# Optimization experiments

Hardware: AMD Instinct MI355X
Metric: run time of the kernel (lower is better)

The kernel has to match this reference:

```python
import jax, jax.numpy as jnp
import numpy as np

CAPACITY_FACTOR = 1.25  # config.capacity_factor


def setup_inputs() -> dict:
    key = jax.random.key(0)
    ks = jax.random.split(key, 5)
    B, S, D, F, E = 8, 2048, 768, 3072, 8
    return {
        "x": jax.random.normal(ks[0], (B, S, D), jnp.float32),
        "switch_w": jax.random.normal(ks[1], (D, E), jnp.float32) * 0.02,
        "switch_b": jnp.zeros((E,), jnp.float32),
        "w1": jax.random.normal(ks[2], (E, D, F), jnp.float32) * 0.02,
        "b1": jnp.zeros((E, F), jnp.float32),
        "w2": jax.random.normal(ks[3], (E, F, D), jnp.float32) * 0.02,
        "b2": jnp.zeros((E, D), jnp.float32),
    }


def reference(x, switch_w, switch_b, w1, b1, w2, b2):
    B, S, D = x.shape
    E = w1.shape[0]
    xf = x.reshape(-1, D)                      # [N, D] tokens
    N = xf.shape[0]
    capacity = int(CAPACITY_FACTOR * N / E)

    # top-1 switch routing
    probs = jax.nn.softmax(xf @ switch_w + switch_b, axis=-1)   # [N, E]
    prob_max = jnp.max(probs, axis=-1)                          # [N]
    routes = jnp.argmax(probs, axis=-1)                         # [N] int

    # priority drop: within each expert keep the `capacity` tokens with
    # highest gate prob. Rank tokens within their expert by descending prob.
    sort_idx = jnp.lexsort((-prob_max, routes))                 # [N]
    counts = jnp.bincount(routes, length=E)
    starts = jnp.concatenate([jnp.zeros((1,), counts.dtype), jnp.cumsum(counts)[:-1]])
    rank_sorted = jnp.arange(N) - starts[routes[sort_idx]]
    rank = jnp.zeros((N,), jnp.int32).at[sort_idx].set(rank_sorted.astype(jnp.int32))
    keep = rank < capacity

    # dispatch kept tokens into [E, capacity, D]; overflow goes to slot E
    dest_e = jnp.where(keep, routes, E)
    dest_c = jnp.where(keep, rank, 0)
    buf = jnp.zeros((E + 1, capacity, D), xf.dtype).at[dest_e, dest_c].set(xf)

    # per-expert FFN (grouped GEMM), GELU is exact (erf) as in nn.GELU()
    h = jax.nn.gelu(jnp.einsum('ecd,edf->ecf', buf[:E], w1) + b1[:, None, :],
                    approximate=False)
    o = jnp.einsum('ecf,efd->ecd', h, w2) + b2[:, None, :]      # [E, cap, D]

    # combine: kept tokens get expert output, dropped tokens pass through x
    y_exp = o[routes, dest_c]                                    # [N, D]
    y = jnp.where(keep[:, None], y_exp, xf)
    out = y * prob_max[:, None]                                  # is_scale_prob
    return out.reshape(B, S, D)
```

## Files before the change

kernel.cpp:

```cpp
#include <hip/hip_runtime.h>
#include <cstdint>
#include <cstddef>

#define E_ 8
#define D_ 768
#define F_ 3072
#define N_ 16384
#define CAP_ 2560
#define NCHUNK_ (N_ / 256)

typedef __attribute__((ext_vector_type(8))) short bf16x8;
typedef __attribute__((ext_vector_type(4))) float f32x4;

__device__ __forceinline__ unsigned short f2bf(float f) {
  unsigned u = __float_as_uint(f);
  u += 0x7fffu + ((u >> 16) & 1u);
  return (unsigned short)(u >> 16);
}

__device__ __forceinline__ void gload16(const void* g, void* l) {
  __builtin_amdgcn_global_load_lds(
      (const __attribute__((address_space(1))) void*)g,
      (__attribute__((address_space(3))) void*)l, 16, 0, 0);
}

__global__ void tcast_kernel(const float* __restrict__ src, unsigned short* __restrict__ dst,
                             int R, int C) {
  __shared__ float tile[64][65];
  int e = blockIdx.z;
  const float* s = src + (size_t)e * R * C;
  unsigned short* d = dst + (size_t)e * R * C;
  int c0 = blockIdx.x * 64, r0 = blockIdx.y * 64;
  int tx = threadIdx.x, ty = threadIdx.y;
  #pragma unroll
  for (int rr = ty; rr < 64; rr += 8) {
    tile[rr][tx]      = s[(size_t)(r0 + rr) * C + c0 + tx];
    tile[rr][tx + 32] = s[(size_t)(r0 + rr) * C + c0 + tx + 32];
  }
  __syncthreads();
  #pragma unroll
  for (int cc = ty; cc < 64; cc += 8) {
    ushort2 o;
    o.x = f2bf(tile[2 * tx][cc]);
    o.y = f2bf(tile[2 * tx + 1][cc]);
    *(ushort2*)&d[(size_t)(c0 + cc) * R + r0 + 2 * tx] = o;
  }
}

__global__ __launch_bounds__(256) void router_kernel(
    const float* __restrict__ x, const float* __restrict__ sw, const float* __restrict__ sb,
    int* __restrict__ route, float* __restrict__ prob,
    unsigned short* __restrict__ xb) {
  __shared__ float wl[E_ * D_];
  int tid = threadIdx.x;
  #pragma unroll
  for (int ee = 0; ee < E_; ++ee)
    for (int dd = tid; dd < D_; dd += 256)
      wl[ee * D_ + dd] = sw[dd * E_ + ee];
  __syncthreads();
  int wave = tid >> 6, lane = tid & 63;
  int tbase = blockIdx.x * 16 + wave * 4;
  #pragma unroll
  for (int tt = 0; tt < 4; ++tt) {
    int t = tbase + tt;
    const float* xp = x + (size_t)t * D_;
    unsigned short* xbp = xb + (size_t)t * D_;
    float acc[E_];
    #pragma unroll
    for (int e = 0; e < E_; ++e) acc[e] = 0.f;
    #pragma unroll
    for (int r = 0; r < D_ / 64; ++r) {
      int dd = r * 64 + lane;
      float xv = xp[dd];
      xbp[dd] = f2bf(xv);
      #pragma unroll
      for (int e = 0; e < E_; ++e) acc[e] += xv * wl[e * D_ + dd];
    }
    #pragma unroll
    for (int e = 0; e < E_; ++e) {
      #pragma unroll
      for (int o = 32; o > 0; o >>= 1) acc[e] += __shfl_xor(acc[e], o);
    }
    if (lane == 0) {
      float mx = -1e30f; int arg = 0;
      #pragma unroll
      for (int e = 0; e < E_; ++e) {
        float l = acc[e] + sb[e];
        acc[e] = l;
        if (l > mx) { mx = l; arg = e; }
      }
      float s = 0.f;
      #pragma unroll
      for (int e = 0; e < E_; ++e) s += expf(acc[e] - mx);
      route[t] = arg;
      prob[t] = 1.f / s;
    }
  }
}

__global__ void hist_kernel(const int* __restrict__ route, int* __restrict__ chunk_hist) {
  __shared__ int h[E_];
  int tid = threadIdx.x;
  if (tid < E_) h[tid] = 0;
  __syncthreads();
  atomicAdd(&h[route[blockIdx.x * 256 + tid]], 1);
  __syncthreads();
  if (tid < E_) chunk_hist[blockIdx.x * E_ + tid] = h[tid];
}

__global__ void scan_kernel(const int* __restrict__ chunk_hist, int* __restrict__ chunk_off,
                            int* __restrict__ counts) {
  __shared__ int h[NCHUNK_ * E_];
  int tid = threadIdx.x;
  h[tid] = chunk_hist[tid];
  __syncthreads();
  if (tid < E_) {
    int run = 0;
    for (int c = 0; c < NCHUNK_; ++c) {
      chunk_off[c * E_ + tid] = run;
      run += h[c * E_ + tid];
    }
    counts[tid] = run;
  }
}

__global__ void assign_kernel(const int* __restrict__ route, const float* __restrict__ prob,
                              const int* __restrict__ counts, const int* __restrict__ chunk_off,
                              int* __restrict__ tok_list, int* __restrict__ slot) {
  __shared__ int rt[256];
  int tid = threadIdx.x;
  int i = blockIdx.x * 256 + tid;
  int e = route[i];
  rt[tid] = e;
  __syncthreads();
  int r = 0;
  for (int j = 0; j < tid; ++j) r += (rt[j] == e) ? 1 : 0;
  int c = counts[e];
  int s; bool keep;
  if (c <= CAP_) {
    s = chunk_off[blockIdx.x * E_ + e] + r;
    keep = true;
  } else {
    float p = prob[i];
    int rr = 0;
    for (int j = 0; j < N_; ++j) {
      if (route[j] == e) {
        float pj = prob[j];
        rr += (pj > p || (pj == p && j < i)) ? 1 : 0;
      }
    }
    s = rr; keep = (rr < CAP_);
  }
  if (keep) tok_list[e * CAP_ + s] = i;
  slot[i] = keep ? s : -1;
}

__global__ __launch_bounds__(256) void gemm1_kernel(
    const unsigned short* __restrict__ xb, const unsigned short* __restrict__ w1t,
    const float* __restrict__ b1, const int* __restrict__ tok_list,
    const int* __restrict__ counts, unsigned short* __restrict__ hb) {
  int e = blockIdx.z;
  int Me = counts[e] < CAP_ ? counts[e] : CAP_;
  int m0 = blockIdx.x * 128;
  if (m0 >= Me) return;
  int n0 = blockIdx.y * 128;
  __shared__ unsigned short At[128 * 32];
  __shared__ unsigned short Bt[128 * 32];
  int tid = threadIdx.x, lane = tid & 63, wave = tid >> 6;
  int rA0 = (wave * 2 + 0) * 16 + (lane >> 2);
  int rA1 = (wave * 2 + 1) * 16 + (lane >> 2);
  int cb = (lane & 3) * 16;
  int mr0 = m0 + rA0; if (mr0 > Me - 1) mr0 = Me - 1;
  int mr1 = m0 + rA1; if (mr1 > Me - 1) mr1 = Me - 1;
  int tok0 = tok_list[e * CAP_ + mr0];
  int tok1 = tok_list[e * CAP_ + mr1];
  const char* gA0 = (const char*)(xb + (size_t)tok0 * D_) + cb;
  const char* gA1 = (const char*)(xb + (size_t)tok1 * D_) + cb;
  const char* gB0 = (const char*)(w1t + ((size_t)e * F_ + n0 + rA0) * D_) + cb;
  const char* gB1 = (const char*)(w1t + ((size_t)e * F_ + n0 + rA1) * D_) + cb;
  unsigned short* lA0 = At + (wave * 2 + 0) * 512;
  unsigned short* lA1 = At + (wave * 2 + 1) * 512;
  unsigned short* lB0 = Bt + (wave * 2 + 0) * 512;
  unsigned short* lB1 = Bt + (wave * 2 + 1) * 512;
  f32x4 acc[4][4] = {};
  int wm = (wave >> 1) * 64, wn = (wave & 1) * 64;
  int fr = lane & 15, fk = (lane >> 4) * 8;
  for (int k0 = 0; k0 < D_; k0 += 32) {
    __syncthreads();
    gload16(gA0 + (size_t)2 * k0, lA0);
    gload16(gA1 + (size_t)2 * k0, lA1);
    gload16(gB0 + (size_t)2 * k0, lB0);
    gload16(gB1 + (size_t)2 * k0, lB1);
    __syncthreads();
    bf16x8 a[4], b[4];
    #pragma unroll
    for (int i = 0; i < 4; ++i)
      a[i] = *(const bf16x8*)(At + (wm + i * 16 + fr) * 32 + fk);
    #pragma unroll
    for (int j = 0; j < 4; ++j)
      b[j] = *(const bf16x8*)(Bt + (wn + j * 16 + fr) * 32 + fk);
    #pragma unroll
    for (int i = 0; i < 4; ++i)
      #pragma unroll
      for (int j = 0; j < 4; ++j)
        acc[i][j] = __builtin_amdgcn_mfma_f32_16x16x32_bf16(a[i], b[j], acc[i][j], 0, 0, 0);
  }
  int q4 = (lane >> 4) * 4;
  #pragma unroll
  for (int i = 0; i < 4; ++i) {
    #pragma unroll
    for (int j = 0; j < 4; ++j) {
      int col = n0 + wn + j * 16 + (lane & 15);
      float bias = b1[e * F_ + col];
      #pragma unroll
      for (int r = 0; r < 4; ++r) {
        int row = m0 + wm + i * 16 + q4 + r;
        if (row < Me) {
          float v = acc[i][j][r] + bias;
          v = 0.5f * v * (1.f + erff(v * 0.70710678118654752f));
          hb[((size_t)e * CAP_ + row) * F_ + col] = f2bf(v);
        }
      }
    }
  }
}

__global__ __launch_bounds__(256) void gemm2_kernel(
    const unsigned short* __restrict__ hb, const unsigned short* __restrict__ w2t,
    const float* __restrict__ b2, const int* __restrict__ tok_list,
    const int* __restrict__ counts, const float* __restrict__ prob,
    float* __restrict__ out) {
  int e = blockIdx.z;
  int Me = counts[e] < CAP_ ? counts[e] : CAP_;
  int m0 = blockIdx.x * 128;
  if (m0 >= Me) return;
  int n0 = blockIdx.y * 128;
  __shared__ unsigned short At[128 * 32];
  __shared__ unsigned short Bt[128 * 32];
  int tid = threadIdx.x, lane = tid & 63, wave = tid >> 6;
  int rA0 = (wave * 2 + 0) * 16 + (lane >> 2);
  int rA1 = (wave * 2 + 1) * 16 + (lane >> 2);
  int cb = (lane & 3) * 16;
  const char* gA0 = (const char*)(hb + ((size_t)e * CAP_ + m0 + rA0) * F_) + cb;
  const char* gA1 = (const char*)(hb + ((size_t)e * CAP_ + m0 + rA1) * F_) + cb;
  const char* gB0 = (const char*)(w2t + ((size_t)e * D_ + n0 + rA0) * F_) + cb;
  const char* gB1 = (const char*)(w2t + ((size_t)e * D_ + n0 + rA1) * F_) + cb;
  unsigned short* lA0 = At + (wave * 2 + 0) * 512;
  unsigned short* lA1 = At + (wave * 2 + 1) * 512;
  unsigned short* lB0 = Bt + (wave * 2 + 0) * 512;
  unsigned short* lB1 = Bt + (wave * 2 + 1) * 512;
  f32x4 acc[4][4] = {};
  int wm = (wave >> 1) * 64, wn = (wave & 1) * 64;
  int fr = lane & 15, fk = (lane >> 4) * 8;
  for (int k0 = 0; k0 < F_; k0 += 32) {
    __syncthreads();
    gload16(gA0 + (size_t)2 * k0, lA0);
    gload16(gA1 + (size_t)2 * k0, lA1);
    gload16(gB0 + (size_t)2 * k0, lB0);
    gload16(gB1 + (size_t)2 * k0, lB1);
    __syncthreads();
    bf16x8 a[4], b[4];
    #pragma unroll
    for (int i = 0; i < 4; ++i)
      a[i] = *(const bf16x8*)(At + (wm + i * 16 + fr) * 32 + fk);
    #pragma unroll
    for (int j = 0; j < 4; ++j)
      b[j] = *(const bf16x8*)(Bt + (wn + j * 16 + fr) * 32 + fk);
    #pragma unroll
    for (int i = 0; i < 4; ++i)
      #pragma unroll
      for (int j = 0; j < 4; ++j)
        acc[i][j] = __builtin_amdgcn_mfma_f32_16x16x32_bf16(a[i], b[j], acc[i][j], 0, 0, 0);
  }
  int q4 = (lane >> 4) * 4;
  #pragma unroll
  for (int i = 0; i < 4; ++i) {
    #pragma unroll
    for (int r = 0; r < 4; ++r) {
      int row = m0 + wm + i * 16 + q4 + r;
      if (row < Me) {
        int tok = tok_list[e * CAP_ + row];
        float pm = prob[tok];
        #pragma unroll
        for (int j = 0; j < 4; ++j) {
          int col = n0 + wn + j * 16 + (lane & 15);
          float v = (acc[i][j][r] + b2[e * D_ + col]) * pm;
          out[(size_t)tok * D_ + col] = v;
        }
      }
    }
  }
}

__global__ void passthrough_kernel(const float* __restrict__ x, const float* __restrict__ prob,
                                   const int* __restrict__ slot, float* __restrict__ out) {
  int t = blockIdx.x;
  if (slot[t] >= 0) return;
  float p = prob[t];
  for (int d = threadIdx.x; d < D_; d += 256)
    out[(size_t)t * D_ + d] = x[(size_t)t * D_ + d] * p;
}

extern "C" void kernel_launch(void* const* d_in, const int* in_sizes, int n_in,
                              void* d_out, int out_size, void* d_ws, size_t ws_size,
                              hipStream_t stream) {
  const float* x  = (const float*)d_in[0];
  const float* sw = (const float*)d_in[1];
  const float* sb = (const float*)d_in[2];
  const float* w1 = (const float*)d_in[3];
  const float* b1 = (const float*)d_in[4];
  const float* w2 = (const float*)d_in[5];
  const float* b2 = (const float*)d_in[6];
  float* out = (float*)d_out;
  (void)in_sizes; (void)n_in; (void)out_size; (void)ws_size;

  char* ws = (char*)d_ws;
  size_t off = 0;
  auto alloc = [&](size_t bytes) {
    char* p = ws + off;
    off = (off + bytes + 255) & ~(size_t)255;
    return p;
  };
  int* counts     = (int*)alloc(32 * sizeof(int));
  int* chunk_hist = (int*)alloc((size_t)NCHUNK_ * E_ * sizeof(int));
  int* chunk_off  = (int*)alloc((size_t)NCHUNK_ * E_ * sizeof(int));
  int* tok_list   = (int*)alloc((size_t)E_ * CAP_ * sizeof(int));
  int* route      = (int*)alloc((size_t)N_ * 4);
  float* prob     = (float*)alloc((size_t)N_ * 4);
  int* slot       = (int*)alloc((size_t)N_ * 4);
  unsigned short* xb  = (unsigned short*)alloc((size_t)N_ * D_ * 2);
  unsigned short* w1t = (unsigned short*)alloc((size_t)E_ * D_ * F_ * 2);
  unsigned short* w2t = (unsigned short*)alloc((size_t)E_ * D_ * F_ * 2);
  unsigned short* hb  = (unsigned short*)alloc((size_t)E_ * CAP_ * F_ * 2);

  dim3 tb(32, 8);
  tcast_kernel<<<dim3(F_ / 64, D_ / 64, E_), tb, 0, stream>>>(w1, w1t, D_, F_);
  tcast_kernel<<<dim3(D_ / 64, F_ / 64, E_), tb, 0, stream>>>(w2, w2t, F_, D_);
  router_kernel<<<N_ / 16, 256, 0, stream>>>(x, sw, sb, route, prob, xb);
  hist_kernel<<<NCHUNK_, 256, 0, stream>>>(route, chunk_hist);
  scan_kernel<<<1, NCHUNK_ * E_, 0, stream>>>(chunk_hist, chunk_off, counts);
  assign_kernel<<<NCHUNK_, 256, 0, stream>>>(route, prob, counts, chunk_off, tok_list, slot);
  gemm1_kernel<<<dim3(CAP_ / 128, F_ / 128, E_), 256, 0, stream>>>(xb, w1t, b1, tok_list, counts, hb);
  gemm2_kernel<<<dim3(CAP_ / 128, D_ / 128, E_), 256, 0, stream>>>(hb, w2t, b2, tok_list, counts, prob, out);
  passthrough_kernel<<<N_, 256, 0, stream>>>(x, prob, slot, out);
}
```

Measured before the change: 590.9 us.

## Double K-tile depth to 64 and XOR-swizzle LDS layout in expert GEMMs

Both grouped GEMM kernels now stage 64-wide K tiles per barrier pair instead of 32, halving the number of synchronizations and load rounds. The global-to-LDS loads are remapped so each 8-lane group covers one 128-byte row, with an XOR swizzle on the 16-byte chunk index, and the fragment reads apply the matching swizzle to avoid LDS bank conflicts. LDS use per block doubles, which may reduce occupancy.

```diff
diff --git a/kernel.cpp b/kernel.cpp
--- a/kernel.cpp
+++ b/kernel.cpp
@@ -155,6 +155,7 @@
   slot[i] = keep ? s : -1;
 }
 
+
 __global__ __launch_bounds__(256) void gemm1_kernel(
     const unsigned short* __restrict__ xb, const unsigned short* __restrict__ w1t,
     const float* __restrict__ b1, const int* __restrict__ tok_list,
@@ -164,46 +165,48 @@
   int m0 = blockIdx.x * 128;
   if (m0 >= Me) return;
   int n0 = blockIdx.y * 128;
-  __shared__ unsigned short At[128 * 32];
-  __shared__ unsigned short Bt[128 * 32];
+  __shared__ unsigned short At[128 * 64];
+  __shared__ unsigned short Bt[128 * 64];
   int tid = threadIdx.x, lane = tid & 63, wave = tid >> 6;
-  int rA0 = (wave * 2 + 0) * 16 + (lane >> 2);
-  int rA1 = (wave * 2 + 1) * 16 + (lane >> 2);
-  int cb = (lane & 3) * 16;
-  int mr0 = m0 + rA0; if (mr0 > Me - 1) mr0 = Me - 1;
-  int mr1 = m0 + rA1; if (mr1 > Me - 1) mr1 = Me - 1;
-  int tok0 = tok_list[e * CAP_ + mr0];
-  int tok1 = tok_list[e * CAP_ + mr1];
-  const char* gA0 = (const char*)(xb + (size_t)tok0 * D_) + cb;
-  const char* gA1 = (const char*)(xb + (size_t)tok1 * D_) + cb;
-  const char* gB0 = (const char*)(w1t + ((size_t)e * F_ + n0 + rA0) * D_) + cb;
-  const char* gB1 = (const char*)(w1t + ((size_t)e * F_ + n0 + rA1) * D_) + cb;
-  unsigned short* lA0 = At + (wave * 2 + 0) * 512;
-  unsigned short* lA1 = At + (wave * 2 + 1) * 512;
-  unsigned short* lB0 = Bt + (wave * 2 + 0) * 512;
-  unsigned short* lB1 = Bt + (wave * 2 + 1) * 512;
+  int lr = lane >> 3;
+  int swb = ((lane & 7) ^ lr) * 16;
+  const char* gA[4]; const char* gB[4];
+  #pragma unroll
+  for (int q = 0; q < 4; ++q) {
+    int mr = m0 + wave * 32 + q * 8 + lr;
+    if (mr > Me - 1) mr = Me - 1;
+    int tok = tok_list[e * CAP_ + mr];
+    gA[q] = (const char*)(xb + (size_t)tok * D_) + swb;
+    int nr = n0 + wave * 32 + q * 8 + lr;
+    gB[q] = (const char*)(w1t + ((size_t)e * F_ + nr) * D_) + swb;
+  }
   f32x4 acc[4][4] = {};
   int wm = (wave >> 1) * 64, wn = (wave & 1) * 64;
-  int fr = lane & 15, fk = (lane >> 4) * 8;
-  for (int k0 = 0; k0 < D_; k0 += 32) {
+  int fr = lane & 15, cg = lane >> 4, s7 = fr & 7;
+  for (int k0 = 0; k0 < D_; k0 += 64) {
     __syncthreads();
-    gload16(gA0 + (size_t)2 * k0, lA0);
-    gload16(gA1 + (size_t)2 * k0, lA1);
-    gload16(gB0 + (size_t)2 * k0, lB0);
-    gload16(gB1 + (size_t)2 * k0, lB1);
+    #pragma unroll
+    for (int q = 0; q < 4; ++q) {
+      gload16(gA[q] + (size_t)2 * k0, At + (wave * 32 + q * 8) * 64);
+      gload16(gB[q] + (size_t)2 * k0, Bt + (wave * 32 + q * 8) * 64);
+    }
     __syncthreads();
-    bf16x8 a[4], b[4];
-    #pragma unroll
-    for (int i = 0; i < 4; ++i)
-      a[i] = *(const bf16x8*)(At + (wm + i * 16 + fr) * 32 + fk);
-    #pragma unroll
-    for (int j = 0; j < 4; ++j)
-      b[j] = *(const bf16x8*)(Bt + (wn + j * 16 + fr) * 32 + fk);
-    #pragma unroll
-    for (int i = 0; i < 4; ++i)
+    #pragma unroll
+    for (int kk = 0; kk < 2; ++kk) {
+      int cp = ((kk * 4 + cg) ^ s7) * 8;
+      bf16x8 a[4], b[4];
+      #pragma unroll
+      for (int i = 0; i < 4; ++i)
+        a[i] = *(const bf16x8*)(At + (wm + i * 16 + fr) * 64 + cp);
       #pragma unroll
       for (int j = 0; j < 4; ++j)
-        acc[i][j] = __builtin_amdgcn_mfma_f32_16x16x32_bf16(a[i], b[j], acc[i][j], 0, 0, 0);
+        b[j] = *(const bf16x8*)(Bt + (wn + j * 16 + fr) * 64 + cp);
+      #pragma unroll
+      for (int i = 0; i < 4; ++i)
+        #pragma unroll
+        for (int j = 0; j < 4; ++j)
+          acc[i][j] = __builtin_amdgcn_mfma_f32_16x16x32_bf16(a[i], b[j], acc[i][j], 0, 0, 0);
+    }
   }
   int q4 = (lane >> 4) * 4;
   #pragma unroll
@@ -235,42 +238,46 @@
   int m0 = blockIdx.x * 128;
   if (m0 >= Me) return;
   int n0 = blockIdx.y * 128;
-  __shared__ unsigned short At[128 * 32];
-  __shared__ unsigned short Bt[128 * 32];
+  __shared__ unsigned short At[128 * 64];
+  __shared__ unsigned short Bt[128 * 64];
   int tid = threadIdx.x, lane = tid & 63, wave = tid >> 6;
-  int rA0 = (wave * 2 + 0) * 16 + (lane >> 2);
-  int rA1 = (wave * 2 + 1) * 16 + (lane >> 2);
-  int cb = (lane & 3) * 16;
-  const char* gA0 = (const char*)(hb + ((size_t)e * CAP_ + m0 + rA0) * F_) + cb;
-  const char* gA1 = (const char*)(hb + ((size_t)e * CAP_ + m0 + rA1) * F_) + cb;
-  const char* gB0 = (const char*)(w2t + ((size_t)e * D_ + n0 + rA0) * F_) + cb;
-  const char* gB1 = (const char*)(w2t + ((size_t)e * D_ + n0 + rA1) * F_) + cb;
-  unsigned short* lA0 = At + (wave * 2 + 0) * 512;
-  unsigned short* lA1 = At + (wave * 2 + 1) * 512;
-  unsigned short* lB0 = Bt + (wave * 2 + 0) * 512;
-  unsigned short* lB1 = Bt + (wave * 2 + 1) * 512;
+  int lr = lane >> 3;
+  int swb = ((lane & 7) ^ lr) * 16;
+  const char* gA[4]; const char* gB[4];
+  #pragma unroll
+  for (int q = 0; q < 4; ++q) {
+    int mr = m0 + wave * 32 + q * 8 + lr;
+    gA[q] = (const char*)(hb + ((size_t)e * CAP_ + mr) * F_) + swb;
+    int nr = n0 + wave * 32 + q * 8 + lr;
+    gB[q] = (const char*)(w2t + ((size_t)e * D_ + nr) * F_) + swb;
+  }
   f32x4 acc[4][4] = {};
   int wm = (wave >> 1) * 64, wn = (wave & 1) * 64;
-  int fr = lane & 15, fk = (lane >> 4) * 8;
-  for (int k0 = 0; k0 < F_; k0 += 32) {
+  int fr = lane & 15, cg = lane >> 4, s7 = fr & 7;
+  for (int k0 = 0; k0 < F_; k0 += 64) {
     __syncthreads();
-    gload16(gA0 + (size_t)2 * k0, lA0);
-    gload16(gA1 + (size_t)2 * k0, lA1);
-    gload16(gB0 + (size_t)2 * k0, lB0);
-    gload16(gB1 + (size_t)2 * k0, lB1);
+    #pragma unroll
+    for (int q = 0; q < 4; ++q) {
+      gload16(gA[q] + (size_t)2 * k0, At + (wave * 32 + q * 8) * 64);
+      gload16(gB[q] + (size_t)2 * k0, Bt + (wave * 32 + q * 8) * 64);
+    }
     __syncthreads();
-    bf16x8 a[4], b[4];
-    #pragma unroll
-    for (int i = 0; i < 4; ++i)
-      a[i] = *(const bf16x8*)(At + (wm + i * 16 + fr) * 32 + fk);
-    #pragma unroll
-    for (int j = 0; j < 4; ++j)
-      b[j] = *(const bf16x8*)(Bt + (wn + j * 16 + fr) * 32 + fk);
-    #pragma unroll
-    for (int i = 0; i < 4; ++i)
+    #pragma unroll
+    for (int kk = 0; kk < 2; ++kk) {
+      int cp = ((kk * 4 + cg) ^ s7) * 8;
+      bf16x8 a[4], b[4];
+      #pragma unroll
+      for (int i = 0; i < 4; ++i)
+        a[i] = *(const bf16x8*)(At + (wm + i * 16 + fr) * 64 + cp);
       #pragma unroll
       for (int j = 0; j < 4; ++j)
-        acc[i][j] = __builtin_amdgcn_mfma_f32_16x16x32_bf16(a[i], b[j], acc[i][j], 0, 0, 0);
+        b[j] = *(const bf16x8*)(Bt + (wn + j * 16 + fr) * 64 + cp);
+      #pragma unroll
+      for (int i = 0; i < 4; ++i)
+        #pragma unroll
+        for (int j = 0; j < 4; ++j)
+          acc[i][j] = __builtin_amdgcn_mfma_f32_16x16x32_bf16(a[i], b[j], acc[i][j], 0, 0, 0);
+    }
   }
   int q4 = (lane >> 4) * 4;
   #pragma unroll
```

After: 624.8 us. 1.06x slower.
